# Performance work log

Hardware: AMD Instinct MI355X
Metric: run time of the kernel (lower is better)

The kernel has to match this reference:

```python
import jax, jax.numpy as jnp
import numpy as np

B, S, D, H, DK = 2, 2048, 1024, 16, 64
NUM_BUCKETS, MAX_DIST = 32, 128
EPS = 1e-6


def _relative_position_bucket(rel, num_buckets=NUM_BUCKETS, max_distance=MAX_DIST):
    # bidirectional (T5 encoder) bucketing
    nb = num_buckets // 2
    bucket = (rel > 0).astype(jnp.int32) * nb
    n = jnp.abs(rel)
    max_exact = nb // 2
    is_small = n < max_exact
    large = max_exact + (
        jnp.log(jnp.maximum(n, 1).astype(jnp.float32) / max_exact)
        / np.log(max_distance / max_exact)
        * (nb - max_exact)
    ).astype(jnp.int32)
    large = jnp.minimum(large, nb - 1)
    return bucket + jnp.where(is_small, n, large)


def softmax1(logits):
    # off-by-one softmax: exp(x-m) / (sum(exp(x-m)) + exp(-m))
    m = jax.lax.stop_gradient(jnp.max(logits, axis=-1, keepdims=True))
    e = jnp.exp(logits - m)
    return e / (jnp.sum(e, axis=-1, keepdims=True) + jnp.exp(-m))


def setup_inputs() -> dict:
    key = jax.random.key(0)
    ks = jax.random.split(key, 8)
    scale = 0.02
    return {
        "hidden_states": jax.random.normal(ks[0], (B, S, D), dtype=jnp.float32),
        "delete_gate_mask": jax.random.normal(ks[1], (B, S, 1), dtype=jnp.float32),
        "ln_w": jnp.ones((D,), dtype=jnp.float32),
        "q_w": jax.random.normal(ks[2], (D, H * DK), dtype=jnp.float32) * scale,
        "k_w": jax.random.normal(ks[3], (D, H * DK), dtype=jnp.float32) * scale,
        "v_w": jax.random.normal(ks[4], (D, H * DK), dtype=jnp.float32) * scale,
        "o_w": jax.random.normal(ks[5], (H * DK, D), dtype=jnp.float32) * scale,
        "rel_emb": jax.random.normal(ks[6], (NUM_BUCKETS, H), dtype=jnp.float32) * scale,
    }


def reference(hidden_states, delete_gate_mask, ln_w, q_w, k_w, v_w, o_w, rel_emb):
    # T5LayerNorm (RMS norm, no mean subtraction, no bias)
    var = jnp.mean(jnp.square(hidden_states), axis=-1, keepdims=True)
    x = hidden_states * jax.lax.rsqrt(var + EPS) * ln_w

    # projections (T5 Linear layers have no bias, no 1/sqrt(d) scaling)
    q = (x @ q_w).reshape(B, S, H, DK).transpose(0, 2, 1, 3)  # bhqd
    k = (x @ k_w).reshape(B, S, H, DK).transpose(0, 2, 1, 3)  # bhkd
    v = (x @ v_w).reshape(B, S, H, DK).transpose(0, 2, 1, 3)  # bhkd

    scores = jnp.einsum("bhqd,bhkd->bhqk", q, k)

    # relative position bias: [1, H, S, S]
    pos = jnp.arange(S)
    rel = pos[None, :] - pos[:, None]  # key_pos - query_pos
    bucket = _relative_position_bucket(rel)  # [S, S]
    position_bias = rel_emb[bucket].transpose(2, 0, 1)[None]  # [1,H,S,S]

    # delete gate: [B,S,1] -> additive mask over key axis [B,1,1,S]
    gate = delete_gate_mask[..., 0][:, None, None, :]

    scores = scores + position_bias + gate
    attn = softmax1(scores.astype(jnp.float32)).astype(scores.dtype)

    attn_out = jnp.einsum("bhqk,bhkd->bhqd", attn, v)
    attn_out = attn_out.transpose(0, 2, 1, 3).reshape(B, S, H * DK) @ o_w

    # residual (dropout disabled at p=0)
    return hidden_states + attn_out
```

## Files before the change

### kernel.cpp

```cpp
#include <hip/hip_runtime.h>
#include <hip/hip_bf16.h>
#include <math.h>

typedef __attribute__((ext_vector_type(8))) short short8;
typedef __attribute__((ext_vector_type(4))) float f32x4;

#define S_LEN   2048
#define DMODEL  1024
#define NHEAD   16
#define HDK     64
#define NBATCH  2
#define MTOT    (NBATCH*S_LEN)
#define LOG2E   1.4426950408889634f

__device__ __forceinline__ unsigned short f2bf(float f) {
  union { float f; unsigned u; } c; c.f = f;
  unsigned r = c.u + 0x7FFFu + ((c.u >> 16) & 1u);
  return (unsigned short)(r >> 16);
}

__device__ __forceinline__ short8 lds_ld16(const unsigned short* p) {
  return *reinterpret_cast<const short8*>(p);
}

__device__ __forceinline__ void gload_lds16(const unsigned short* g, unsigned short* l) {
  __builtin_amdgcn_global_load_lds(
      (const __attribute__((address_space(1))) unsigned int*)g,
      (__attribute__((address_space(3))) unsigned int*)l, 16, 0, 0);
}

__global__ __launch_bounds__(256) void fused_prep_kernel(
    const float* __restrict__ hs, const float* __restrict__ lnw,
    const float* __restrict__ rel_emb, const float* __restrict__ gmask,
    const float* __restrict__ qw, const float* __restrict__ kw,
    const float* __restrict__ vw, const float* __restrict__ ow,
    unsigned short* __restrict__ xo, float* __restrict__ btab,
    float* __restrict__ egf, unsigned short* __restrict__ egb,
    unsigned short* __restrict__ wqkv, unsigned short* __restrict__ wo) {
  const int blk = blockIdx.x, t = threadIdx.x;
  if (blk < MTOT) {
    const int row = blk;
    const float4 v = ((const float4*)(hs + (size_t)row*DMODEL))[t];
    float ss = v.x*v.x + v.y*v.y + v.z*v.z + v.w*v.w;
    #pragma unroll
    for (int off = 32; off >= 1; off >>= 1) ss += __shfl_xor(ss, off, 64);
    __shared__ float wsum[4];
    if ((t & 63) == 0) wsum[t >> 6] = ss;
    __syncthreads();
    float tot = wsum[0] + wsum[1] + wsum[2] + wsum[3];
    float sc = rsqrtf(tot * (1.0f/DMODEL) + 1e-6f);
    const float4 lw = ((const float4*)lnw)[t];
    uint2 o;
    o.x = (unsigned)f2bf(v.x*sc*lw.x) | ((unsigned)f2bf(v.y*sc*lw.y) << 16);
    o.y = (unsigned)f2bf(v.z*sc*lw.z) | ((unsigned)f2bf(v.w*sc*lw.w) << 16);
    ((uint2*)(xo + (size_t)row*DMODEL))[t] = o;
  } else if (blk < MTOT + 4096) {
    int bb = blk - MTOT;
    int z = bb >> 10, rem = bb & 1023;
    const float* src = (z==0)?qw:(z==1)?kw:(z==2)?vw:ow;
    unsigned short* dst = (z<3) ? (wqkv + (size_t)z*DMODEL*DMODEL) : wo;
    __shared__ float tile[32][33];
    int n0 = (rem & 31)*32, k0 = (rem >> 5)*32;
    int tx = t & 31, ty = t >> 5;
    for (int r = ty; r < 32; r += 8)
      tile[r][tx] = src[(size_t)(k0+r)*DMODEL + n0 + tx];
    __syncthreads();
    for (int r = ty; r < 32; r += 8)
      dst[(size_t)(n0+r)*DMODEL + k0 + tx] = f2bf(tile[tx][r]);
  } else if (blk < MTOT + 4096 + 256) {
    int idx = (blk - MTOT - 4096)*256 + t;
    if (idx >= NHEAD*4095) return;
    int h = idx / 4095, rp = idx % 4095, rel = rp - 2047;
    int bucket = (rel > 0) ? 16 : 0;
    int n = (rel < 0) ? -rel : rel;
    int v;
    if (n < 8) v = n;
    else {
      float lrv = logf((float)n * 0.125f) / 2.7725887f * 8.0f;
      v = 8 + (int)lrv;
      if (v > 15) v = 15;
    }
    btab[idx] = rel_emb[(size_t)(bucket + v)*NHEAD + h] * LOG2E;
  } else {
    int i = (blk - MTOT - 4096 - 256)*256 + t;
    float e = __expf(gmask[i]);
    egf[i] = e;
    egb[i] = f2bf(e);
  }
}

template<int EPI>
__global__ __launch_bounds__(256) void gemm128(
    const unsigned short* __restrict__ X,
    const unsigned short* __restrict__ W,
    unsigned short* __restrict__ Oq, unsigned short* __restrict__ Ok,
    unsigned short* __restrict__ Ov,
    const float* __restrict__ resid, float* __restrict__ Of,
    const float* __restrict__ escale) {
  __shared__ unsigned short As[128*64];
  __shared__ unsigned short Bs[128*64];
  const int z = blockIdx.z;
  int m0, n0;
  const unsigned short *Ap, *Bp;
  if (EPI == 0 && z == 2) {
    m0 = blockIdx.y*128; n0 = blockIdx.x*128;
    Ap = W + (size_t)2*DMODEL*DMODEL; Bp = X;
  } else {
    m0 = blockIdx.x*128; n0 = blockIdx.y*128;
    Ap = X; Bp = W + ((EPI==0) ? (size_t)z*DMODEL*DMODEL : 0);
  }
  const int t = threadIdx.x, lane = t & 63, w = t >> 6;
  const int g = lane >> 4, lr = lane & 15;
  const int wr = (w >> 1)*64, wc = (w & 1)*64;

  f32x4 acc[4][4];
  #pragma unroll
  for (int mi = 0; mi < 4; mi++)
    #pragma unroll
    for (int ni = 0; ni < 4; ni++) acc[mi][ni] = (f32x4){0.f,0.f,0.f,0.f};

  const unsigned short* ag[4]; const unsigned short* bg[4];
  unsigned short* al[4]; unsigned short* bl[4];
  #pragma unroll
  for (int i = 0; i < 4; i++) {
    int slot = t + i*256, row = slot >> 3, c8 = slot & 7;
    int cs = c8 ^ (row & 7);
    ag[i] = Ap + (size_t)(m0 + row)*DMODEL + cs*8;
    bg[i] = Bp + (size_t)(n0 + row)*DMODEL + cs*8;
    al[i] = As + slot*8;
    bl[i] = Bs + slot*8;
  }

  for (int kk = 0; kk < DMODEL; kk += 64) {
    #pragma unroll
    for (int i = 0; i < 4; i++) {
      gload_lds16(ag[i] + kk, al[i]);
      gload_lds16(bg[i] + kk, bl[i]);
    }
    __syncthreads();
    #pragma unroll
    for (int ks = 0; ks < 2; ks++) {
      short8 af[4], bfr[4];
      #pragma unroll
      for (int mi = 0; mi < 4; mi++) {
        int R = wr + mi*16 + lr;
        af[mi] = lds_ld16(As + R*64 + (((ks*4 + g) ^ (R & 7)) << 3));
      }
      #pragma unroll
      for (int ni = 0; ni < 4; ni++) {
        int R = wc + ni*16 + lr;
        bfr[ni] = lds_ld16(Bs + R*64 + (((ks*4 + g) ^ (R & 7)) << 3));
      }
      #pragma unroll
      for (int mi = 0; mi < 4; mi++)
        #pragma unroll
        for (int ni = 0; ni < 4; ni++)
          acc[mi][ni] = __builtin_amdgcn_mfma_f32_16x16x32_bf16(af[mi], bfr[ni], acc[mi][ni], 0, 0, 0);
    }
    __syncthreads();
  }

  if (EPI == 0) {
    if (z < 2) {
      unsigned short* dst = (z == 0) ? Oq : Ok;
      const float osc = (z == 0) ? LOG2E : 1.0f;
      #pragma unroll
      for (int mi = 0; mi < 4; mi++) {
        #pragma unroll
        for (int r = 0; r < 4; r++) {
          int m = m0 + wr + mi*16 + g*4 + r;
          int b = m >> 11, s = m & (S_LEN-1);
          unsigned short* drow = dst + ((size_t)b*NHEAD*S_LEN + s)*HDK;
          #pragma unroll
          for (int ni = 0; ni < 4; ni++) {
            int n = n0 + wc + ni*16 + lr;
            int h = n >> 6, dcol = n & 63;
            drow[(size_t)h*S_LEN*HDK + dcol] = f2bf(acc[mi][ni][r] * osc);
          }
        }
      }
    } else {
      #pragma unroll
      for (int ni = 0; ni < 4; ni++) {
        int n = n0 + wc + ni*16 + lr;
        int b = n >> 11, s = n & (S_LEN-1);
        float e = escale[n];
        #pragma unroll
        for (int mi = 0; mi < 4; mi++)
          #pragma unroll
          for (int r = 0; r < 4; r++) {
            int m = m0 + wr + mi*16 + g*4 + r;
            Ov[((size_t)b*DMODEL + m)*S_LEN + s] = f2bf(acc[mi][ni][r] * e);
          }
      }
    }
  } else {
    #pragma unroll
    for (int mi = 0; mi < 4; mi++) {
      #pragma unroll
      for (int r = 0; r < 4; r++) {
        int m = m0 + wr + mi*16 + g*4 + r;
        const float* rrow = resid + (size_t)m*DMODEL;
        float* orow = Of + (size_t)m*DMODEL;
        #pragma unroll
        for (int ni = 0; ni < 4; ni++) {
          int n = n0 + wc + ni*16 + lr;
          orow[n] = rrow[n] + acc[mi][ni][r];
        }
      }
    }
  }
}

__global__ __launch_bounds__(256, 2) void attn_kernel(
    const unsigned short* __restrict__ Qg,
    const unsigned short* __restrict__ Kg,
    const unsigned short* __restrict__ Vtg,
    const float* __restrict__ btab,
    const unsigned short* __restrict__ egb,
    unsigned short* __restrict__ Og) {
  __shared__ __align__(16) unsigned short Kl[2][64][64];
  __shared__ __align__(16) unsigned short Vl[2][64][64];
  __shared__ __align__(16) unsigned short Pl[4][16*64];

  const int flat = blockIdx.x;
  const int xcd = flat & 7, j = flat >> 3;
  const int bh = xcd*4 + (j >> 4), qx = j & 15;
  const int b = bh >> 4, h = bh & 15;
  const int q0 = qx * 128;

  const int t = threadIdx.x, w = t >> 6, lane = t & 63;
  const int g = lane >> 4, lr = lane & 15, l7 = lane & 7;
  const int srow0 = t >> 3, sg0 = t & 7, srow1 = srow0 + 32;
  const int swz = (sg0 ^ (srow0 & 7)) << 3;

  const unsigned short* Qb = Qg  + (size_t)bh*S_LEN*HDK;
  const unsigned short* Kb = Kg  + (size_t)bh*S_LEN*HDK;
  const unsigned short* Vb = Vtg + (size_t)bh*HDK*S_LEN;
  const unsigned short* ge = egb + (size_t)b*S_LEN;

  const int qs0A = q0 + w*32, qs0B = qs0A + 16;
  short8 qfA0 = *reinterpret_cast<const short8*>(Qb + (size_t)(qs0A+lr)*HDK + g*8);
  short8 qfA1 = *reinterpret_cast<const short8*>(Qb + (size_t)(qs0A+lr)*HDK + 32 + g*8);
  short8 qfB0 = *reinterpret_cast<const short8*>(Qb + (size_t)(qs0B+lr)*HDK + g*8);
  short8 qfB1 = *reinterpret_cast<const short8*>(Qb + (size_t)(qs0B+lr)*HDK + 32 + g*8);

  f32x4 accA[4], accB[4], l4A, l4B;
  #pragma unroll
  for (int n = 0; n < 4; n++) { accA[n] = (f32x4){0.f,0.f,0.f,0.f}; accB[n] = (f32x4){0.f,0.f,0.f,0.f}; }
  l4A = (f32x4){0.f,0.f,0.f,0.f}; l4B = (f32x4){0.f,0.f,0.f,0.f};

  const float* btb = btab + (size_t)h*4095 + 2047;
  const float cpos = btb[91];
  const float cneg = btb[-91];

  {
    *reinterpret_cast<uint4*>(&Kl[0][srow0][swz]) =
        *reinterpret_cast<const uint4*>(Kb + (size_t)srow0*HDK + sg0*8);
    *reinterpret_cast<uint4*>(&Kl[0][srow1][swz]) =
        *reinterpret_cast<const uint4*>(Kb + (size_t)srow1*HDK + sg0*8);
    *reinterpret_cast<uint4*>(&Vl[0][srow0][swz]) =
        *reinterpret_cast<const uint4*>(Vb + (size_t)srow0*S_LEN + sg0*8);
    *reinterpret_cast<uint4*>(&Vl[0][srow1][swz]) =
        *reinterpret_cast<const uint4*>(Vb + (size_t)srow1*S_LEN + sg0*8);
  }

  char* prow = (char*)&Pl[w][0] + lr*128;

  int cur = 0;
  const int NT = S_LEN/64;
  for (int kt = 0; kt < NT; ++kt) {
    const int key0 = kt*64;
    __syncthreads();

    uint4 nk0, nk1, nv0, nv1;
    const bool pf = (kt + 1 < NT);
    if (pf) {
      nk0 = *reinterpret_cast<const uint4*>(Kb + (size_t)(key0+64+srow0)*HDK + sg0*8);
      nk1 = *reinterpret_cast<const uint4*>(Kb + (size_t)(key0+64+srow1)*HDK + sg0*8);
      nv0 = *reinterpret_cast<const uint4*>(Vb + (size_t)srow0*S_LEN + key0+64 + sg0*8);
      nv1 = *reinterpret_cast<const uint4*>(Vb + (size_t)srow1*S_LEN + key0+64 + sg0*8);
    }

    short8 bk[4][2];
    #pragma unroll
    for (int n = 0; n < 4; n++) {
      const unsigned short* kr = &Kl[cur][n*16 + lr][0];
      bk[n][0] = lds_ld16(kr + ((g ^ l7) << 3));
      bk[n][1] = lds_ld16(kr + (((4 + g) ^ l7) << 3));
    }
    short8 bv[2][4];
    #pragma unroll
    for (int c = 0; c < 2; c++)
      #pragma unroll
      for (int n = 0; n < 4; n++)
        bv[c][n] = lds_ld16(&Vl[cur][n*16 + lr][((4*c + g) ^ l7) << 3]);
    short8 gv[2];
    #pragma unroll
    for (int c = 0; c < 2; c++) {
      short8 z8 = (short8){0,0,0,0,0,0,0,0};
      if (lr == 0)
        z8 = *reinterpret_cast<const short8*>(ge + key0 + c*32 + g*8);
      gv[c] = z8;
    }

#define PROCESS_SET(qf0_, qf1_, qs0_, acc_, l4_)                                      \
    {                                                                                 \
      const int dband = key0 - (qs0_);                                                \
      const bool band = (dband > -154 && dband < 106);                                \
      const float cc = band ? 0.f : ((dband > 0) ? cpos : cneg);                      \
      f32x4 zc = (f32x4){cc, cc, cc, cc};               \
      f32x4 sv[4];                                                                    \
      __builtin_amdgcn_s_setprio(1);                                                  \
      _Pragma("unroll") for (int n = 0; n < 4; n++) {                                 \
        sv[n] = __builtin_amdgcn_mfma_f32_16x16x32_bf16(bk[n][0], qf0_, zc, 0, 0, 0); \
        sv[n] = __builtin_amdgcn_mfma_f32_16x16x32_bf16(bk[n][1], qf1_, sv[n], 0, 0, 0); \
      }                                                                               \
      __builtin_amdgcn_s_setprio(0);                                                  \
      if (band) {                                                                     \
        const float* btq = btb + (dband - lr);                                        \
        _Pragma("unroll") for (int n = 0; n < 4; n++)                                 \
          _Pragma("unroll") for (int r = 0; r < 4; r++)                               \
            sv[n][r] += btq[n*16 + g*4 + r];                                          \
      }                                                                               \
      _Pragma("unroll") for (int n = 0; n < 4; n++)                                   \
        _Pragma("unroll") for (int r = 0; r < 4; r++)                                 \
          sv[n][r] = exp2f(sv[n][r]);                                                 \
      _Pragma("unroll") for (int n = 0; n < 4; n++) {                                 \
        unsigned plo_, phi_;                                                          \
        asm("v_cvt_pk_bf16_f32 %0, %1, %2" : "=v"(plo_) : "v"(sv[n][0]), "v"(sv[n][1])); \
        asm("v_cvt_pk_bf16_f32 %0, %1, %2" : "=v"(phi_) : "v"(sv[n][2]), "v"(sv[n][3])); \
        uint2 pw_; pw_.x = plo_; pw_.y = phi_;                                        \
        *reinterpret_cast<uint2*>(prow + ((((2*n + (g>>1)) ^ l7) << 4) + ((g & 1) << 3))) = pw_; \
      }                                                                               \
      __builtin_amdgcn_s_setprio(1);                                                  \
      _Pragma("unroll") for (int c = 0; c < 2; c++) {                                 \
        short8 pa_ = lds_ld16((const unsigned short*)(prow + (((4*c + g) ^ l7) << 4))); \
        _Pragma("unroll") for (int n = 0; n < 4; n++)                                 \
          acc_[n] = __builtin_amdgcn_mfma_f32_16x16x32_bf16(pa_, bv[c][n], acc_[n], 0, 0, 0); \
        l4_ = __builtin_amdgcn_mfma_f32_16x16x32_bf16(pa_, gv[c], l4_, 0, 0, 0);      \
      }                                                                               \
      __builtin_amdgcn_s_setprio(0);                                                  \
    }

    PROCESS_SET(qfA0, qfA1, qs0A, accA, l4A)
    PROCESS_SET(qfB0, qfB1, qs0B, accB, l4B)
#undef PROCESS_SET

    if (pf) {
      *reinterpret_cast<uint4*>(&Kl[cur^1][srow0][swz]) = nk0;
      *reinterpret_cast<uint4*>(&Kl[cur^1][srow1][swz]) = nk1;
      *reinterpret_cast<uint4*>(&Vl[cur^1][srow0][swz]) = nv0;
      *reinterpret_cast<uint4*>(&Vl[cur^1][srow1][swz]) = nv1;
    }
    cur ^= 1;
  }

#define FINAL_SET(acc_, l4_, qs0_)                                                    \
  {                                                                                   \
    _Pragma("unroll") for (int r = 0; r < 4; r++) {                                   \
      float lq = __shfl(l4_[r], g*16);                                                \
      float inv = 1.0f / (lq + 1.0f);                                                 \
      int srw = (qs0_) + g*4 + r;                                                     \
      unsigned short* orow = Og + ((size_t)b*S_LEN + srw)*DMODEL + h*HDK;             \
      _Pragma("unroll") for (int n = 0; n < 4; n++)                                   \
        orow[n*16 + lr] = f2bf(acc_[n][r] * inv);                                     \
    }                                                                                 \
  }
  FINAL_SET(accA, l4A, qs0A)
  FINAL_SET(accB, l4B, qs0B)
#undef FINAL_SET
}

extern "C" void kernel_launch(void* const* d_in, const int* in_sizes, int n_in,
                              void* d_out, int out_size, void* d_ws, size_t ws_size,
                              hipStream_t stream) {
  const float* hs   = (const float*)d_in[0];
  const float* gate = (const float*)d_in[1];
  const float* lnw  = (const float*)d_in[2];
  const float* qw   = (const float*)d_in[3];
  const float* kw   = (const float*)d_in[4];
  const float* vw   = (const float*)d_in[5];
  const float* ow   = (const float*)d_in[6];
  const float* rel  = (const float*)d_in[7];
  float* out = (float*)d_out;

  char* ws = (char*)d_ws;
  const size_t MB = 1ull << 20;
  unsigned short* xbf  = (unsigned short*)(ws);
  unsigned short* wqkv = (unsigned short*)(ws + 8*MB);
  unsigned short* wo   = (unsigned short*)(ws + 14*MB);
  unsigned short* qb   = (unsigned short*)(ws + 16*MB);
  unsigned short* kb   = (unsigned short*)(ws + 24*MB);
  unsigned short* vt   = (unsigned short*)(ws + 32*MB);
  unsigned short* ao   = (unsigned short*)(ws + 40*MB);
  float*          btab = (float*)(ws + 48*MB);
  float*          egf  = (float*)(ws + 48*MB + 256*1024);
  unsigned short* egb  = (unsigned short*)(ws + 48*MB + 272*1024);

  fused_prep_kernel<<<dim3(MTOT + 4096 + 256 + 16), dim3(256), 0, stream>>>(
      hs, lnw, rel, gate, qw, kw, vw, ow, xbf, btab, egf, egb, wqkv, wo);
  gemm128<0><<<dim3(MTOT/128, DMODEL/128, 3), dim3(256), 0, stream>>>(
      xbf, wqkv, qb, kb, vt, nullptr, nullptr, egf);
  attn_kernel<<<dim3(512), dim3(256), 0, stream>>>(
      qb, kb, vt, btab, egb, ao);
  gemm128<1><<<dim3(MTOT/128, DMODEL/128, 1), dim3(256), 0, stream>>>(
      ao, wo, nullptr, nullptr, nullptr, hs, out, nullptr);
}
```

Before: 133.3 us.

## Use 256x128 tiles with 512 threads for QKV projection GEMM

Splits the templated GEMM in two. The QKV projection gets a 256x128 tile with 8 waves, and the output projection keeps the 128x128 kernel. The larger M tile raises reuse of each B tile and halves the block count. The V branch remaps blocks so they cover the transposed 1024x4096 output, and the MFMA section is wrapped in s_setprio. The cost is more LDS per block (48KB) and fewer blocks in flight, which may hurt occupancy or tail balance.

```diff
diff --git a/kernel.cpp b/kernel.cpp
--- a/kernel.cpp
+++ b/kernel.cpp
@@ -89,26 +89,125 @@
   }
 }
 
-template<int EPI>
-__global__ __launch_bounds__(256) void gemm128(
+__global__ __launch_bounds__(512) void gemm256(
     const unsigned short* __restrict__ X,
     const unsigned short* __restrict__ W,
     unsigned short* __restrict__ Oq, unsigned short* __restrict__ Ok,
     unsigned short* __restrict__ Ov,
-    const float* __restrict__ resid, float* __restrict__ Of,
     const float* __restrict__ escale) {
-  __shared__ unsigned short As[128*64];
+  __shared__ unsigned short As[256*64];
   __shared__ unsigned short Bs[128*64];
   const int z = blockIdx.z;
   int m0, n0;
   const unsigned short *Ap, *Bp;
-  if (EPI == 0 && z == 2) {
-    m0 = blockIdx.y*128; n0 = blockIdx.x*128;
+  if (z == 2) {
+    int flat = blockIdx.x + 16*blockIdx.y;
+    m0 = (flat & 3)*256; n0 = (flat >> 2)*128;
     Ap = W + (size_t)2*DMODEL*DMODEL; Bp = X;
   } else {
-    m0 = blockIdx.x*128; n0 = blockIdx.y*128;
-    Ap = X; Bp = W + ((EPI==0) ? (size_t)z*DMODEL*DMODEL : 0);
-  }
+    m0 = blockIdx.x*256; n0 = blockIdx.y*128;
+    Ap = X; Bp = W + (size_t)z*DMODEL*DMODEL;
+  }
+  const int t = threadIdx.x, lane = t & 63, w = t >> 6;
+  const int g = lane >> 4, lr = lane & 15;
+  const int wr = (w >> 1)*64, wc = (w & 1)*64;
+
+  f32x4 acc[4][4];
+  #pragma unroll
+  for (int mi = 0; mi < 4; mi++)
+    #pragma unroll
+    for (int ni = 0; ni < 4; ni++) acc[mi][ni] = (f32x4){0.f,0.f,0.f,0.f};
+
+  const unsigned short* ag[4]; unsigned short* al[4];
+  #pragma unroll
+  for (int i = 0; i < 4; i++) {
+    int slot = t + i*512, row = slot >> 3, c8 = slot & 7;
+    int cs = c8 ^ (row & 7);
+    ag[i] = Ap + (size_t)(m0 + row)*DMODEL + cs*8;
+    al[i] = As + slot*8;
+  }
+  const unsigned short* bg[2]; unsigned short* bl[2];
+  #pragma unroll
+  for (int i = 0; i < 2; i++) {
+    int slot = t + i*512, row = slot >> 3, c8 = slot & 7;
+    int cs = c8 ^ (row & 7);
+    bg[i] = Bp + (size_t)(n0 + row)*DMODEL + cs*8;
+    bl[i] = Bs + slot*8;
+  }
+
+  for (int kk = 0; kk < DMODEL; kk += 64) {
+    #pragma unroll
+    for (int i = 0; i < 4; i++) gload_lds16(ag[i] + kk, al[i]);
+    #pragma unroll
+    for (int i = 0; i < 2; i++) gload_lds16(bg[i] + kk, bl[i]);
+    __syncthreads();
+    #pragma unroll
+    for (int ks = 0; ks < 2; ks++) {
+      short8 af[4], bfr[4];
+      #pragma unroll
+      for (int mi = 0; mi < 4; mi++) {
+        int R = wr + mi*16 + lr;
+        af[mi] = lds_ld16(As + R*64 + (((ks*4 + g) ^ (R & 7)) << 3));
+      }
+      #pragma unroll
+      for (int ni = 0; ni < 4; ni++) {
+        int R = wc + ni*16 + lr;
+        bfr[ni] = lds_ld16(Bs + R*64 + (((ks*4 + g) ^ (R & 7)) << 3));
+      }
+      __builtin_amdgcn_s_setprio(1);
+      #pragma unroll
+      for (int mi = 0; mi < 4; mi++)
+        #pragma unroll
+        for (int ni = 0; ni < 4; ni++)
+          acc[mi][ni] = __builtin_amdgcn_mfma_f32_16x16x32_bf16(af[mi], bfr[ni], acc[mi][ni], 0, 0, 0);
+      __builtin_amdgcn_s_setprio(0);
+    }
+    __syncthreads();
+  }
+
+  if (z < 2) {
+    unsigned short* dst = (z == 0) ? Oq : Ok;
+    const float osc = (z == 0) ? LOG2E : 1.0f;
+    #pragma unroll
+    for (int mi = 0; mi < 4; mi++) {
+      #pragma unroll
+      for (int r = 0; r < 4; r++) {
+        int m = m0 + wr + mi*16 + g*4 + r;
+        int b = m >> 11, s = m & (S_LEN-1);
+        unsigned short* drow = dst + ((size_t)b*NHEAD*S_LEN + s)*HDK;
+        #pragma unroll
+        for (int ni = 0; ni < 4; ni++) {
+          int n = n0 + wc + ni*16 + lr;
+          int h = n >> 6, dcol = n & 63;
+          drow[(size_t)h*S_LEN*HDK + dcol] = f2bf(acc[mi][ni][r] * osc);
+        }
+      }
+    }
+  } else {
+    #pragma unroll
+    for (int ni = 0; ni < 4; ni++) {
+      int n = n0 + wc + ni*16 + lr;
+      int b = n >> 11, s = n & (S_LEN-1);
+      float e = escale[n];
+      #pragma unroll
+      for (int mi = 0; mi < 4; mi++)
+        #pragma unroll
+        for (int r = 0; r < 4; r++) {
+          int m = m0 + wr + mi*16 + g*4 + r;
+          Ov[((size_t)b*DMODEL + m)*S_LEN + s] = f2bf(acc[mi][ni][r] * e);
+        }
+    }
+  }
+}
+
+__global__ __launch_bounds__(256) void gemm128o(
+    const unsigned short* __restrict__ X,
+    const unsigned short* __restrict__ W,
+    const float* __restrict__ resid, float* __restrict__ Of) {
+  __shared__ unsigned short As[128*64];
+  __shared__ unsigned short Bs[128*64];
+  const int m0 = blockIdx.x*128, n0 = blockIdx.y*128;
+  const unsigned short *Ap = X, *Bp = W;
   const int t = threadIdx.x, lane = t & 63, w = t >> 6;
   const int g = lane >> 4, lr = lane & 15;
   const int wr = (w >> 1)*64, wc = (w & 1)*64;
@@ -160,53 +259,17 @@
     __syncthreads();
   }
 
-  if (EPI == 0) {
-    if (z < 2) {
-      unsigned short* dst = (z == 0) ? Oq : Ok;
-      const float osc = (z == 0) ? LOG2E : 1.0f;
-      #pragma unroll
-      for (int mi = 0; mi < 4; mi++) {
-        #pragma unroll
-        for (int r = 0; r < 4; r++) {
-          int m = m0 + wr + mi*16 + g*4 + r;
-          int b = m >> 11, s = m & (S_LEN-1);
-          unsigned short* drow = dst + ((size_t)b*NHEAD*S_LEN + s)*HDK;
-          #pragma unroll
-          for (int ni = 0; ni < 4; ni++) {
-            int n = n0 + wc + ni*16 + lr;
-            int h = n >> 6, dcol = n & 63;
-            drow[(size_t)h*S_LEN*HDK + dcol] = f2bf(acc[mi][ni][r] * osc);
-          }
-        }
-      }
-    } else {
+  #pragma unroll
+  for (int mi = 0; mi < 4; mi++) {
+    #pragma unroll
+    for (int r = 0; r < 4; r++) {
+      int m = m0 + wr + mi*16 + g*4 + r;
+      const float* rrow = resid + (size_t)m*DMODEL;
+      float* orow = Of + (size_t)m*DMODEL;
       #pragma unroll
       for (int ni = 0; ni < 4; ni++) {
         int n = n0 + wc + ni*16 + lr;
-        int b = n >> 11, s = n & (S_LEN-1);
-        float e = escale[n];
-        #pragma unroll
-        for (int mi = 0; mi < 4; mi++)
-          #pragma unroll
-          for (int r = 0; r < 4; r++) {
-            int m = m0 + wr + mi*16 + g*4 + r;
-            Ov[((size_t)b*DMODEL + m)*S_LEN + s] = f2bf(acc[mi][ni][r] * e);
-          }
-      }
-    }
-  } else {
-    #pragma unroll
-    for (int mi = 0; mi < 4; mi++) {
-      #pragma unroll
-      for (int r = 0; r < 4; r++) {
-        int m = m0 + wr + mi*16 + g*4 + r;
-        const float* rrow = resid + (size_t)m*DMODEL;
-        float* orow = Of + (size_t)m*DMODEL;
-        #pragma unroll
-        for (int ni = 0; ni < 4; ni++) {
-          int n = n0 + wc + ni*16 + lr;
-          orow[n] = rrow[n] + acc[mi][ni][r];
-        }
+        orow[n] = rrow[n] + acc[mi][ni][r];
       }
     }
   }
@@ -400,10 +463,10 @@
 
   fused_prep_kernel<<<dim3(MTOT + 4096 + 256 + 16), dim3(256), 0, stream>>>(
       hs, lnw, rel, gate, qw, kw, vw, ow, xbf, btab, egf, egb, wqkv, wo);
-  gemm128<0><<<dim3(MTOT/128, DMODEL/128, 3), dim3(256), 0, stream>>>(
-      xbf, wqkv, qb, kb, vt, nullptr, nullptr, egf);
+  gemm256<<<dim3(MTOT/256, DMODEL/128, 3), dim3(512), 0, stream>>>(
+      xbf, wqkv, qb, kb, vt, egf);
   attn_kernel<<<dim3(512), dim3(256), 0, stream>>>(
       qb, kb, vt, btab, egb, ao);
-  gemm128<1><<<dim3(MTOT/128, DMODEL/128, 1), dim3(256), 0, stream>>>(
-      ao, wo, nullptr, nullptr, nullptr, hs, out, nullptr);
-}
+  gemm128o<<<dim3(MTOT/128, DMODEL/128), dim3(256), 0, stream>>>(
+      ao, wo, hs, out);
+}
```

Result: slower. 145.4 us (+9.0%).

## Interleave QK, softmax and PV phases of the two query sets

Applied to the files above, without the earlier changes.

Issues the QK^T MFMAs for both 16-row query sets together, then interleaves the exp/pack work of set B with the PV MFMAs of set A. P now gets a separate LDS buffer per set, so the two pack stores and reads no longer share one region. The goal is to overlap the VALU exp work with matrix-core work inside each wavefront. In exchange, more registers hold live scores (svA and svB at once), which may raise pressure at launch bounds (256,2), and LDS use grows.

```diff
diff --git a/kernel.cpp b/kernel.cpp
--- a/kernel.cpp
+++ b/kernel.cpp
@@ -221,7 +221,7 @@
     unsigned short* __restrict__ Og) {
   __shared__ __align__(16) unsigned short Kl[2][64][64];
   __shared__ __align__(16) unsigned short Vl[2][64][64];
-  __shared__ __align__(16) unsigned short Pl[4][16*64];
+  __shared__ __align__(16) unsigned short Pl[4][2][16*64];
 
   const int flat = blockIdx.x;
   const int xcd = flat & 7, j = flat >> 3;
@@ -265,7 +265,8 @@
         *reinterpret_cast<const uint4*>(Vb + (size_t)srow1*S_LEN + sg0*8);
   }
 
-  char* prow = (char*)&Pl[w][0] + lr*128;
+  char* prowA = (char*)&Pl[w][0][0] + lr*128;
+  char* prowB = (char*)&Pl[w][1][0] + lr*128;
 
   int cur = 0;
   const int NT = S_LEN/64;
@@ -304,55 +305,78 @@
       gv[c] = z8;
     }
 
-#define PROCESS_SET(qf0_, qf1_, qs0_, acc_, l4_)                                      \
+    const int dbA = key0 - qs0A, dbB = key0 - qs0B;
+    const bool bandA = (dbA > -154 && dbA < 106);
+    const bool bandB = (dbB > -154 && dbB < 106);
+    const float ccA = bandA ? 0.f : ((dbA > 0) ? cpos : cneg);
+    const float ccB = bandB ? 0.f : ((dbB > 0) ? cpos : cneg);
+    f32x4 svA[4], svB[4];
+    {
+      f32x4 zA = (f32x4){ccA,ccA,ccA,ccA}, zB = (f32x4){ccB,ccB,ccB,ccB};
+      __builtin_amdgcn_s_setprio(1);
+      #pragma unroll
+      for (int n = 0; n < 4; n++) {
+        svA[n] = __builtin_amdgcn_mfma_f32_16x16x32_bf16(bk[n][0], qfA0, zA, 0, 0, 0);
+        svB[n] = __builtin_amdgcn_mfma_f32_16x16x32_bf16(bk[n][0], qfB0, zB, 0, 0, 0);
+      }
+      #pragma unroll
+      for (int n = 0; n < 4; n++) {
+        svA[n] = __builtin_amdgcn_mfma_f32_16x16x32_bf16(bk[n][1], qfA1, svA[n], 0, 0, 0);
+        svB[n] = __builtin_amdgcn_mfma_f32_16x16x32_bf16(bk[n][1], qfB1, svB[n], 0, 0, 0);
+      }
+      __builtin_amdgcn_s_setprio(0);
+    }
+
+#define SM_PHASE(sv_, band_, db_)                                                     \
     {                                                                                 \
-      const int dband = key0 - (qs0_);                                                \
-      const bool band = (dband > -154 && dband < 106);                                \
-      const float cc = band ? 0.f : ((dband > 0) ? cpos : cneg);                      \
-      f32x4 zc = (f32x4){cc, cc, cc, cc};               \
-      f32x4 sv[4];                                                                    \
-      __builtin_amdgcn_s_setprio(1);                                                  \
-      _Pragma("unroll") for (int n = 0; n < 4; n++) {                                 \
-        sv[n] = __builtin_amdgcn_mfma_f32_16x16x32_bf16(bk[n][0], qf0_, zc, 0, 0, 0); \
-        sv[n] = __builtin_amdgcn_mfma_f32_16x16x32_bf16(bk[n][1], qf1_, sv[n], 0, 0, 0); \
-      }                                                                               \
-      __builtin_amdgcn_s_setprio(0);                                                  \
-      if (band) {                                                                     \
-        const float* btq = btb + (dband - lr);                                        \
+      if (band_) {                                                                    \
+        const float* btq = btb + ((db_) - lr);                                        \
         _Pragma("unroll") for (int n = 0; n < 4; n++)                                 \
           _Pragma("unroll") for (int r = 0; r < 4; r++)                               \
-            sv[n][r] += btq[n*16 + g*4 + r];                                          \
+            sv_[n][r] += btq[n*16 + g*4 + r];                                         \
       }                                                                               \
       _Pragma("unroll") for (int n = 0; n < 4; n++)                                   \
         _Pragma("unroll") for (int r = 0; r < 4; r++)                                 \
-          sv[n][r] = exp2f(sv[n][r]);                                                 \
+          sv_[n][r] = exp2f(sv_[n][r]);                                               \
+    }
+#define PACK_PHASE(sv_, prow_)                                                        \
+    {                                                                                 \
       _Pragma("unroll") for (int n = 0; n < 4; n++) {                                 \
         unsigned plo_, phi_;                                                          \
-        asm("v_cvt_pk_bf16_f32 %0, %1, %2" : "=v"(plo_) : "v"(sv[n][0]), "v"(sv[n][1])); \
-        asm("v_cvt_pk_bf16_f32 %0, %1, %2" : "=v"(phi_) : "v"(sv[n][2]), "v"(sv[n][3])); \
+        asm("v_cvt_pk_bf16_f32 %0, %1, %2" : "=v"(plo_) : "v"(sv_[n][0]), "v"(sv_[n][1])); \
+        asm("v_cvt_pk_bf16_f32 %0, %1, %2" : "=v"(phi_) : "v"(sv_[n][2]), "v"(sv_[n][3])); \
         uint2 pw_; pw_.x = plo_; pw_.y = phi_;                                        \
-        *reinterpret_cast<uint2*>(prow + ((((2*n + (g>>1)) ^ l7) << 4) + ((g & 1) << 3))) = pw_; \
+        *reinterpret_cast<uint2*>((prow_) + ((((2*n + (g>>1)) ^ l7) << 4) + ((g & 1) << 3))) = pw_; \
       }                                                                               \
-      __builtin_amdgcn_s_setprio(1);                                                  \
+    }
+#define PV_PHASE(prow_, acc_, l4_)                                                    \
+    {                                                                                 \
       _Pragma("unroll") for (int c = 0; c < 2; c++) {                                 \
-        short8 pa_ = lds_ld16((const unsigned short*)(prow + (((4*c + g) ^ l7) << 4))); \
+        short8 pa_ = lds_ld16((const unsigned short*)((prow_) + (((4*c + g) ^ l7) << 4))); \
+        __builtin_amdgcn_s_setprio(1);                                                \
         _Pragma("unroll") for (int n = 0; n < 4; n++)                                 \
           acc_[n] = __builtin_amdgcn_mfma_f32_16x16x32_bf16(pa_, bv[c][n], acc_[n], 0, 0, 0); \
         l4_ = __builtin_amdgcn_mfma_f32_16x16x32_bf16(pa_, gv[c], l4_, 0, 0, 0);      \
+        __builtin_amdgcn_s_setprio(0);                                                \
       }                                                                               \
-      __builtin_amdgcn_s_setprio(0);                                                  \
-    }
-
-    PROCESS_SET(qfA0, qfA1, qs0A, accA, l4A)
-    PROCESS_SET(qfB0, qfB1, qs0B, accB, l4B)
-#undef PROCESS_SET
-
+    }
+
+    SM_PHASE(svA, bandA, dbA)
+    PACK_PHASE(svA, prowA)
+    SM_PHASE(svB, bandB, dbB)
+    PV_PHASE(prowA, accA, l4A)
+    PACK_PHASE(svB, prowB)
     if (pf) {
       *reinterpret_cast<uint4*>(&Kl[cur^1][srow0][swz]) = nk0;
       *reinterpret_cast<uint4*>(&Kl[cur^1][srow1][swz]) = nk1;
       *reinterpret_cast<uint4*>(&Vl[cur^1][srow0][swz]) = nv0;
       *reinterpret_cast<uint4*>(&Vl[cur^1][srow1][swz]) = nv1;
     }
+    PV_PHASE(prowB, accB, l4B)
+#undef SM_PHASE
+#undef PACK_PHASE
+#undef PV_PHASE
+
     cur ^= 1;
   }
 
```

New measurement: 134.2 us. No clear change (+0.7%).
